# Optimization experiments

Hardware: AMD Instinct MI355X
Metric: run time of the kernel (lower is better)

Reference implementation:

```python
import jax, jax.numpy as jnp
import numpy as np

B, C, W, H, HEADS = 4, 512, 32, 32, 8
D = C // HEADS          # head dim = 64
N = W * H               # tokens = 1024


def setup_inputs() -> dict:
    key = jax.random.key(0)
    ks = jax.random.split(key, 11)
    s = 0.02
    return {
        "q1": jax.random.normal(ks[0], (B, C, W, H), jnp.float32),
        "q2": jax.random.normal(ks[1], (B, C, W, H), jnp.float32),
        "q3": jax.random.normal(ks[2], (B, C, W, H), jnp.float32),
        "Wq": jax.random.normal(ks[3], (C, C), jnp.float32) * s,
        "bq": jnp.zeros((C,), jnp.float32),
        "Wk": jax.random.normal(ks[4], (C, C), jnp.float32) * s,
        "bk": jnp.zeros((C,), jnp.float32),
        "Wv": jax.random.normal(ks[5], (C, C), jnp.float32) * s,
        "bv": jnp.zeros((C,), jnp.float32),
        # BoT-style relative position embeddings (broadcast over the grid)
        "rel_h": jax.random.normal(ks[6], (HEADS, D, 1, H), jnp.float32) * s,
        "rel_w": jax.random.normal(ks[7], (HEADS, D, W, 1), jnp.float32) * s,
    }


def reference(q1, q2, q3, Wq, bq, Wk, bk, Wv, bv, rel_h, rel_w):
    b, c, w, h = q1.shape
    heads = rel_h.shape[0]
    d = c // heads
    n = w * h

    def proj(x, Wm, bm):
        # 1x1 conv == channel matmul; then view (b, heads, d, n)
        y = jnp.einsum('oc,bchw->bohw', Wm, x) + bm[None, :, None, None]
        return y.reshape(b, heads, d, n)

    q = proj(q1, Wq, bq)
    k = proj(q2, Wk, bk)
    v = proj(q3, Wv, bv)

    # (heads, d, w, h) -> (heads, d, n); used transposed as (heads, n, d)
    pos = (rel_h + rel_w).reshape(heads, d, n)

    def branch(a, bmat, outv):
        # energy = a^T bmat + pos^T a ; softmax over last dim; out = outv @ attn^T
        energy = (jnp.einsum('bhdn,bhdm->bhnm', a, bmat)
                  + jnp.einsum('hdn,bhdm->bhnm', pos, a))
        attn = jax.nn.softmax(energy, axis=-1)  # (b, heads, n, n)
        out = jnp.einsum('bhdm,bhnm->bhdn', outv, attn)
        return out.reshape(b, c, w, h)

    out_q = branch(q, k, v)   # energy_q = q^T k + pos^T q ; out = v @ attn_q^T
    out_k = branch(k, v, q)   # energy_k = k^T v + pos^T k ; out = q @ attn_k^T
    out_v = branch(v, q, k)   # energy_v = v^T q + pos^T v ; out = k @ attn_v^T

    return jnp.concatenate((out_q, out_k, out_v), axis=0)
```

## Files before the change

kernel.cpp:

```cpp
#include <hip/hip_runtime.h>

typedef __attribute__((ext_vector_type(8))) __bf16 bf16x8;
typedef __attribute__((ext_vector_type(4))) float f32x4;
typedef __attribute__((ext_vector_type(4))) int i32x4;
typedef __attribute__((ext_vector_type(2))) int i32x2;
typedef __attribute__((ext_vector_type(4))) unsigned short u16x4;
typedef __attribute__((ext_vector_type(8))) unsigned short u16x8;
typedef unsigned short u16;
typedef unsigned int u32;

#define DEVI __device__ __forceinline__

constexpr int CB = 4;
constexpr int CC = 512;
constexpr int CH = 8;
constexpr int CD = 64;
constexpr int CN = 1024;
constexpr float L2E = 1.44269504088896f;

DEVI u16 f2bf(float f) {
    u32 u = __builtin_bit_cast(u32, f);
    u = (u + 0x7FFFu + ((u >> 16) & 1u)) >> 16;
    return (u16)u;
}
DEVI float bf2f(u16 u) {
    return __builtin_bit_cast(float, (u32)u << 16);
}
DEVI u16 f2bf_c(float f) {
    return __builtin_bit_cast(u16, (__bf16)f);
}
DEVI float exp2_fast(float x) {
    float r;
    asm("v_exp_f32 %0, %1" : "=v"(r) : "v"(x));
    return r;
}

DEVI int swzA(int row, int col16) {
    return (row * 256 + col16 * 16) ^ ((row & 7) << 4);
}
DEVI int swzB(int row, int col16) {
    return (row * 128 + col16 * 16) ^ ((row & 7) << 4);
}

DEVI bf16x8 ldfrag(const u16* base, int byteoff) {
    const i32x4* p = reinterpret_cast<const i32x4*>(reinterpret_cast<const char*>(base) + byteoff);
    return __builtin_bit_cast(bf16x8, *p);
}
DEVI void st16(u16* base, int byteoff, i32x4 v) {
    *reinterpret_cast<i32x4*>(reinterpret_cast<char*>(base) + byteoff) = v;
}
DEVI void st8(u16* base, int byteoff, i32x2 v) {
    *reinterpret_cast<i32x2*>(reinterpret_cast<char*>(base) + byteoff) = v;
}
DEVI void async16(u16* lds, const u16* g) {
    __builtin_amdgcn_global_load_lds(
        (const __attribute__((address_space(1))) unsigned int*)g,
        (__attribute__((address_space(3))) unsigned int*)lds,
        16, 0, 0);
}

__global__ __launch_bounds__(256) void mqf_convx_kernel(
    const float* __restrict__ q1, const float* __restrict__ q2, const float* __restrict__ q3,
    u16* __restrict__ XT)
{
    __shared__ u16 T[64 * 66];
    const int t = threadIdx.x;
    const int n0 = blockIdx.x * 64, c0 = blockIdx.y * 64;
    const int p = blockIdx.z >> 2, b = blockIdx.z & 3;
    const float* X = (p == 0 ? q1 : p == 1 ? q2 : q3) + (size_t)b * CC * CN;
    u16* dst = XT + (size_t)(p * CB + b) * CN * CC;

    #pragma unroll
    for (int pass = 0; pass < 4; ++pass) {
        int idx = pass * 256 + t;
        int cl = idx >> 4, nl = (idx & 15) * 4;
        f32x4 v = *reinterpret_cast<const f32x4*>(X + (size_t)(c0 + cl) * CN + n0 + nl);
        u32 lo = (u32)f2bf(v[0]) | ((u32)f2bf(v[1]) << 16);
        u32 hi = (u32)f2bf(v[2]) | ((u32)f2bf(v[3]) << 16);
        *reinterpret_cast<u32*>(&T[cl * 66 + nl]) = lo;
        *reinterpret_cast<u32*>(&T[cl * 66 + nl + 2]) = hi;
    }
    __syncthreads();
    #pragma unroll
    for (int pass = 0; pass < 2; ++pass) {
        int idx = pass * 256 + t;
        int nl = idx >> 3, g = idx & 7;
        u16x8 pk;
        #pragma unroll
        for (int j = 0; j < 8; ++j) pk[j] = T[(g * 8 + j) * 66 + nl];
        *reinterpret_cast<u16x8*>(dst + (size_t)(n0 + nl) * CC + c0 + g * 8) = pk;
    }
}

__global__ __launch_bounds__(256) void mqf_convw_kernel(
    const float* __restrict__ Wq, const float* __restrict__ Wk, const float* __restrict__ Wv,
    u16* __restrict__ Wbf)
{
    int idx = (blockIdx.x * 256 + threadIdx.x) * 4;
    int p = idx >> 18;
    int off = idx & 0x3FFFF;
    const float* W = (p == 0 ? Wq : p == 1 ? Wk : Wv);
    f32x4 v = *reinterpret_cast<const f32x4*>(W + off);
    u16x4 pk;
    #pragma unroll
    for (int j = 0; j < 4; ++j) pk[j] = f2bf(v[j]);
    *reinterpret_cast<u16x4*>(Wbf + idx) = pk;
}

__global__ __launch_bounds__(256) void mqf_gemm_kernel(
    const u16* __restrict__ Wbf, const u16* __restrict__ XT,
    const float* __restrict__ bq, const float* __restrict__ bk, const float* __restrict__ bv,
    u16* __restrict__ projN, u16* __restrict__ projT)
{
    __shared__ __align__(16) u16 At[128 * 64];
    __shared__ __align__(16) u16 Bt[128 * 64];

    const int t = threadIdx.x;
    const int w = t >> 6, l = t & 63;
    const int n0 = blockIdx.x * 128;
    const int o0 = blockIdx.y * 128;
    const int p = blockIdx.z >> 2, b = blockIdx.z & 3;

    const u16* A = Wbf + (size_t)p * CC * CC;
    const u16* B = XT + (size_t)(p * CB + b) * CN * CC;
    const float* bm = (p == 0 ? bq : p == 1 ? bk : bv);
    u16* oN = projN + (size_t)(p * CB + b) * CC * CN;
    u16* oT = projT + (size_t)(p * CB + b) * CN * CC;

    const int srow = t >> 3;
    const int sj = t & 7;

    const f32x4 fz = {0.f, 0.f, 0.f, 0.f};
    f32x4 acc[4][4];
    #pragma unroll
    for (int m = 0; m < 4; ++m)
        #pragma unroll
        for (int s = 0; s < 4; ++s) acc[m][s] = fz;

    const int wr = (w >> 1) * 64;
    const int wc = (w & 1) * 64;

    for (int c0 = 0; c0 < CC; c0 += 64) {
        __syncthreads();
        #pragma unroll
        for (int q = 0; q < 4; ++q) {
            int row = q * 32 + srow;
            int col = (sj ^ (row & 7)) * 8;
            async16(&At[q * 2048 + t * 8], A + (size_t)(o0 + row) * CC + c0 + col);
            async16(&Bt[q * 2048 + t * 8], B + (size_t)(n0 + row) * CC + c0 + col);
        }
        __syncthreads();
        __builtin_amdgcn_s_setprio(1);
        #pragma unroll
        for (int kk = 0; kk < 2; ++kk) {
            bf16x8 af[4], bfr[4];
            #pragma unroll
            for (int m = 0; m < 4; ++m)
                af[m] = ldfrag(At, swzB(wr + m * 16 + (l & 15), kk * 4 + (l >> 4)));
            #pragma unroll
            for (int s = 0; s < 4; ++s)
                bfr[s] = ldfrag(Bt, swzB(wc + s * 16 + (l & 15), kk * 4 + (l >> 4)));
            #pragma unroll
            for (int m = 0; m < 4; ++m)
                #pragma unroll
                for (int s = 0; s < 4; ++s)
                    acc[m][s] = __builtin_amdgcn_mfma_f32_16x16x32_bf16(af[m], bfr[s], acc[m][s], 0, 0, 0);
        }
        __builtin_amdgcn_s_setprio(0);
    }

    #pragma unroll
    for (int m = 0; m < 4; ++m) {
        int obase = o0 + wr + m * 16 + (l >> 4) * 4;
        float bias[4];
        #pragma unroll
        for (int r = 0; r < 4; ++r) bias[r] = bm[obase + r];
        #pragma unroll
        for (int s = 0; s < 4; ++s) {
            int n = n0 + wc + s * 16 + (l & 15);
            u16x4 pk;
            #pragma unroll
            for (int r = 0; r < 4; ++r) {
                float v = acc[m][s][r] + bias[r];
                pk[r] = f2bf(v);
                oN[(size_t)(obase + r) * CN + n] = pk[r];
            }
            *reinterpret_cast<u16x4*>(oT + (size_t)n * CC + obase) = pk;
        }
    }
}

__global__ __launch_bounds__(256, 3) void mqf_attn_kernel(
    const u16* __restrict__ projN, const u16* __restrict__ projT,
    const float* __restrict__ rel_h, const float* __restrict__ rel_w,
    float* __restrict__ out)
{
    __shared__ __align__(16) u16 Kt[2][64 * 128];
    __shared__ __align__(16) u16 Vt[2][64 * 64];

    const int t = threadIdx.x;
    const int w = t >> 6, l = t & 63;
    const int li = l & 15, hi = l >> 4;

    int id = blockIdx.x + (blockIdx.y << 3) + (blockIdx.z << 8);
    int nid = (id & 7) * 96 + (id >> 3);
    const int n0 = (nid & 7) * 128;
    const int by = (nid >> 3) & 31;
    const int br = nid >> 8;
    const int b = by >> 3, h = by & 7;

    const int ai = br, bi = (br + 1) % 3, vi = (br + 2) % 3;
    const size_t tsz = (size_t)CB * CC * CN;
    const u16* aT = projT + ai * tsz + (size_t)b * CN * CC;
    const u16* bT = projT + bi * tsz + (size_t)b * CN * CC;
    const u16* vN = projN + vi * tsz + (size_t)b * CC * CN;

    bf16x8 qf[2][4];
    #pragma unroll
    for (int g = 0; g < 2; ++g) {
        const int nq = n0 + (w * 2 + g) * 16 + li;
        #pragma unroll
        for (int kk = 0; kk < 2; ++kk) {
            u16x8 raw = *reinterpret_cast<const u16x8*>(
                aT + (size_t)nq * CC + h * CD + kk * 32 + hi * 8);
            u16x8 pk;
            #pragma unroll
            for (int j = 0; j < 8; ++j) pk[j] = f2bf_c(bf2f(raw[j]) * L2E);
            qf[g][kk] = __builtin_bit_cast(bf16x8, pk);
        }
        #pragma unroll
        for (int kk = 2; kk < 4; ++kk) {
            u16x8 pk;
            #pragma unroll
            for (int j = 0; j < 8; ++j) {
                int d = (kk - 2) * 32 + hi * 8 + j;
                float f = rel_h[(h * CD + d) * 32 + (nq & 31)]
                        + rel_w[(h * CD + d) * 32 + (nq >> 5)];
                pk[j] = f2bf_c(f * L2E);
            }
            qf[g][kk] = __builtin_bit_cast(bf16x8, pk);
        }
    }

    const f32x4 fz = {0.f, 0.f, 0.f, 0.f};
    f32x4 oacc[2][4];
    #pragma unroll
    for (int g = 0; g < 2; ++g)
        #pragma unroll
        for (int dg = 0; dg < 4; ++dg) oacc[g][dg] = fz;
    float lsum[2] = {0.f, 0.f};

    i32x4 kreg[4], vreg[2];
    const int krow = t >> 2, kc = (t & 3) * 8;
    const int vrow = t >> 3, vc = (t & 7) * 8;
    const int k7 = krow & 7;
    const int vb0 = ((vc >> 5) << 6) + (((vc >> 2) & 3) << 4) + (((vc >> 4) & 1) << 3);

    auto loadKV = [&](int m1) {
        const u16* rb = bT + (size_t)(m1 + krow) * CC + h * CD;
        const u16* ra = aT + (size_t)(m1 + krow) * CC + h * CD;
        kreg[0] = *reinterpret_cast<const i32x4*>(rb + kc);
        kreg[1] = *reinterpret_cast<const i32x4*>(rb + 32 + kc);
        kreg[2] = *reinterpret_cast<const i32x4*>(ra + kc);
        kreg[3] = *reinterpret_cast<const i32x4*>(ra + 32 + kc);
        const u16* rv = vN + (size_t)(h * CD + vrow) * CN + m1;
        vreg[0] = *reinterpret_cast<const i32x4*>(rv + vc);
        vreg[1] = *reinterpret_cast<const i32x4*>(rv + (size_t)32 * CN + vc);
    };
    auto writeKV = [&](u16* KtW, u16* VtW) {
        #pragma unroll
        for (int q = 0; q < 4; ++q) {
            int u = q * 4 + (t & 3);
            st16(KtW, krow * 256 + ((u ^ k7) << 4), kreg[q]);
        }
        i32x2 lo0 = {vreg[0][0], vreg[0][1]}, hi0 = {vreg[0][2], vreg[0][3]};
        int r0 = vrow, r1 = vrow + 32;
        st8(VtW, (r0 * 128 + vb0) ^ ((r0 & 7) << 4), lo0);
        st8(VtW, (r0 * 128 + vb0 + 16) ^ ((r0 & 7) << 4), hi0);
        i32x2 lo1 = {vreg[1][0], vreg[1][1]}, hi1 = {vreg[1][2], vreg[1][3]};
        st8(VtW, (r1 * 128 + vb0) ^ ((r1 & 7) << 4), lo1);
        st8(VtW, (r1 * 128 + vb0 + 16) ^ ((r1 & 7) << 4), hi1);
    };

    loadKV(0);
    writeKV(Kt[0], Vt[0]);
    loadKV(64);
    __syncthreads();

    for (int tt = 0; tt < 16; ++tt) {
        const u16* KtC = Kt[tt & 1];
        const u16* VtC = Vt[tt & 1];
        if (tt < 15) writeKV(Kt[(tt + 1) & 1], Vt[(tt + 1) & 1]);
        if (tt < 14) loadKV((tt + 2) * 64);

        f32x4 e[2][4];
        #pragma unroll
        for (int s = 0; s < 4; ++s) { e[0][s] = fz; e[1][s] = fz; }
        __builtin_amdgcn_s_setprio(1);
        #pragma unroll
        for (int kk = 0; kk < 4; ++kk) {
            #pragma unroll
            for (int s = 0; s < 4; ++s) {
                bf16x8 af = ldfrag(KtC, swzA(s * 16 + li, kk * 4 + hi));
                e[0][s] = __builtin_amdgcn_mfma_f32_16x16x32_bf16(af, qf[0][kk], e[0][s], 0, 0, 0);
                e[1][s] = __builtin_amdgcn_mfma_f32_16x16x32_bf16(af, qf[1][kk], e[1][s], 0, 0, 0);
            }
        }
        __builtin_amdgcn_s_setprio(0);

        bf16x8 pa[2][2];
        #pragma unroll
        for (int g = 0; g < 2; ++g) {
            float ts = 0.f;
            #pragma unroll
            for (int s = 0; s < 4; ++s) {
                #pragma unroll
                for (int r = 0; r < 4; ++r) {
                    float pv = exp2_fast(e[g][s][r]);
                    e[g][s][r] = pv;
                    ts += pv;
                }
            }
            lsum[g] += ts;
            #pragma unroll
            for (int kk = 0; kk < 2; ++kk) {
                u16x8 pk;
                #pragma unroll
                for (int r = 0; r < 4; ++r) {
                    pk[r]     = f2bf_c(e[g][2 * kk][r]);
                    pk[4 + r] = f2bf_c(e[g][2 * kk + 1][r]);
                }
                pa[g][kk] = __builtin_bit_cast(bf16x8, pk);
            }
        }

        __builtin_amdgcn_s_setprio(1);
        #pragma unroll
        for (int kk = 0; kk < 2; ++kk) {
            #pragma unroll
            for (int dg = 0; dg < 4; ++dg) {
                bf16x8 vf = ldfrag(VtC, swzB(dg * 16 + li, kk * 4 + hi));
                oacc[0][dg] = __builtin_amdgcn_mfma_f32_16x16x32_bf16(vf, pa[0][kk], oacc[0][dg], 0, 0, 0);
                oacc[1][dg] = __builtin_amdgcn_mfma_f32_16x16x32_bf16(vf, pa[1][kk], oacc[1][dg], 0, 0, 0);
            }
        }
        __builtin_amdgcn_s_setprio(0);
        __syncthreads();
    }

    #pragma unroll
    for (int g = 0; g < 2; ++g) {
        float lt = lsum[g];
        lt += __shfl_xor(lt, 16, 64);
        lt += __shfl_xor(lt, 32, 64);
        float inv = 1.f / lt;
        float* outp = out + ((size_t)(br * CB + b) * CC + h * CD) * CN
                    + n0 + (w * 2 + g) * 16 + li;
        #pragma unroll
        for (int dg = 0; dg < 4; ++dg) {
            #pragma unroll
            for (int r = 0; r < 4; ++r) {
                int drow = dg * 16 + hi * 4 + r;
                outp[(size_t)drow * CN] = oacc[g][dg][r] * inv;
            }
        }
    }
}

extern "C" void kernel_launch(void* const* d_in, const int* in_sizes, int n_in,
                              void* d_out, int out_size, void* d_ws, size_t ws_size,
                              hipStream_t stream) {
    const float* q1 = (const float*)d_in[0];
    const float* q2 = (const float*)d_in[1];
    const float* q3 = (const float*)d_in[2];
    const float* Wq = (const float*)d_in[3];
    const float* bq = (const float*)d_in[4];
    const float* Wk = (const float*)d_in[5];
    const float* bk = (const float*)d_in[6];
    const float* Wv = (const float*)d_in[7];
    const float* bv = (const float*)d_in[8];
    const float* rh = (const float*)d_in[9];
    const float* rw = (const float*)d_in[10];

    u16* XT    = (u16*)d_ws;
    u16* Wbf   = XT + (size_t)3 * CB * CN * CC;
    u16* projN = Wbf + (size_t)3 * CC * CC;
    u16* projT = projN + (size_t)3 * CB * CC * CN;
    float* outp = (float*)d_out;

    dim3 gc(CN / 64, CC / 64, 12);
    mqf_convx_kernel<<<gc, 256, 0, stream>>>(q1, q2, q3, XT);
    mqf_convw_kernel<<<768, 256, 0, stream>>>(Wq, Wk, Wv, Wbf);
    dim3 gg(CN / 128, CC / 128, 12);
    mqf_gemm_kernel<<<gg, 256, 0, stream>>>(Wbf, XT, bq, bk, bv, projN, projT);
    dim3 ga(CN / 128, CB * CH, 3);
    mqf_attn_kernel<<<ga, 256, 0, stream>>>(projN, projT, rh, rw, outp);
}
```

Baseline: 82.39 us.

## Software-pipeline PV MFMA of previous tile behind current QK and softmax

Splits the K and V staging into separate load/write steps and delays V's shared-memory write by one iteration. The P·V matrix multiply for tile tt-1 is issued right after the QK MFMAs of tile tt, inside the same high-priority region. A final epilogue handles the last tile. The aim is to overlap the exp/convert softmax work with MFMA execution and to shorten the critical path between the two matmul phases. The cost is that the pa fragments stay live across iterations, which raises register pressure.

New measurement: 86.37 us. 1.05x slower.

```diff
diff --git a/kernel.cpp b/kernel.cpp
--- a/kernel.cpp
+++ b/kernel.cpp
@@ -249,6 +249,7 @@
         #pragma unroll
         for (int dg = 0; dg < 4; ++dg) oacc[g][dg] = fz;
     float lsum[2] = {0.f, 0.f};
+    bf16x8 pa[2][2];
 
     i32x4 kreg[4], vreg[2];
     const int krow = t >> 2, kc = (t & 3) * 8;
@@ -256,23 +257,27 @@
     const int k7 = krow & 7;
     const int vb0 = ((vc >> 5) << 6) + (((vc >> 2) & 3) << 4) + (((vc >> 4) & 1) << 3);
 
-    auto loadKV = [&](int m1) {
+    auto loadK = [&](int m1) {
         const u16* rb = bT + (size_t)(m1 + krow) * CC + h * CD;
         const u16* ra = aT + (size_t)(m1 + krow) * CC + h * CD;
         kreg[0] = *reinterpret_cast<const i32x4*>(rb + kc);
         kreg[1] = *reinterpret_cast<const i32x4*>(rb + 32 + kc);
         kreg[2] = *reinterpret_cast<const i32x4*>(ra + kc);
         kreg[3] = *reinterpret_cast<const i32x4*>(ra + 32 + kc);
+    };
+    auto loadV = [&](int m1) {
         const u16* rv = vN + (size_t)(h * CD + vrow) * CN + m1;
         vreg[0] = *reinterpret_cast<const i32x4*>(rv + vc);
         vreg[1] = *reinterpret_cast<const i32x4*>(rv + (size_t)32 * CN + vc);
     };
-    auto writeKV = [&](u16* KtW, u16* VtW) {
+    auto writeK = [&](u16* KtW) {
         #pragma unroll
         for (int q = 0; q < 4; ++q) {
             int u = q * 4 + (t & 3);
             st16(KtW, krow * 256 + ((u ^ k7) << 4), kreg[q]);
         }
+    };
+    auto writeV = [&](u16* VtW) {
         i32x2 lo0 = {vreg[0][0], vreg[0][1]}, hi0 = {vreg[0][2], vreg[0][3]};
         int r0 = vrow, r1 = vrow + 32;
         st8(VtW, (r0 * 128 + vb0) ^ ((r0 & 7) << 4), lo0);
@@ -282,16 +287,19 @@
         st8(VtW, (r1 * 128 + vb0 + 16) ^ ((r1 & 7) << 4), hi1);
     };
 
-    loadKV(0);
-    writeKV(Kt[0], Vt[0]);
-    loadKV(64);
+    loadK(0);
+    loadV(0);
+    writeK(Kt[0]);
+    loadK(64);
     __syncthreads();
 
     for (int tt = 0; tt < 16; ++tt) {
+        writeV(Vt[tt & 1]);
+        if (tt < 15) writeK(Kt[(tt + 1) & 1]);
+        if (tt < 14) loadK((tt + 2) * 64);
+        if (tt < 15) loadV((tt + 1) * 64);
+
         const u16* KtC = Kt[tt & 1];
-        const u16* VtC = Vt[tt & 1];
-        if (tt < 15) writeKV(Kt[(tt + 1) & 1], Vt[(tt + 1) & 1]);
-        if (tt < 14) loadKV((tt + 2) * 64);
 
         f32x4 e[2][4];
         #pragma unroll
@@ -306,9 +314,20 @@
                 e[1][s] = __builtin_amdgcn_mfma_f32_16x16x32_bf16(af, qf[1][kk], e[1][s], 0, 0, 0);
             }
         }
+        if (tt > 0) {
+            const u16* VtP = Vt[(tt - 1) & 1];
+            #pragma unroll
+            for (int kk = 0; kk < 2; ++kk) {
+                #pragma unroll
+                for (int dg = 0; dg < 4; ++dg) {
+                    bf16x8 vf = ldfrag(VtP, swzB(dg * 16 + li, kk * 4 + hi));
+                    oacc[0][dg] = __builtin_amdgcn_mfma_f32_16x16x32_bf16(vf, pa[0][kk], oacc[0][dg], 0, 0, 0);
+                    oacc[1][dg] = __builtin_amdgcn_mfma_f32_16x16x32_bf16(vf, pa[1][kk], oacc[1][dg], 0, 0, 0);
+                }
+            }
+        }
         __builtin_amdgcn_s_setprio(0);
 
-        bf16x8 pa[2][2];
         #pragma unroll
         for (int g = 0; g < 2; ++g) {
             float ts = 0.f;
@@ -333,20 +352,20 @@
                 pa[g][kk] = __builtin_bit_cast(bf16x8, pk);
             }
         }
-
-        __builtin_amdgcn_s_setprio(1);
-        #pragma unroll
-        for (int kk = 0; kk < 2; ++kk) {
-            #pragma unroll
-            for (int dg = 0; dg < 4; ++dg) {
-                bf16x8 vf = ldfrag(VtC, swzB(dg * 16 + li, kk * 4 + hi));
-                oacc[0][dg] = __builtin_amdgcn_mfma_f32_16x16x32_bf16(vf, pa[0][kk], oacc[0][dg], 0, 0, 0);
-                oacc[1][dg] = __builtin_amdgcn_mfma_f32_16x16x32_bf16(vf, pa[1][kk], oacc[1][dg], 0, 0, 0);
-            }
-        }
-        __builtin_amdgcn_s_setprio(0);
         __syncthreads();
     }
+
+    __builtin_amdgcn_s_setprio(1);
+    #pragma unroll
+    for (int kk = 0; kk < 2; ++kk) {
+        #pragma unroll
+        for (int dg = 0; dg < 4; ++dg) {
+            bf16x8 vf = ldfrag(Vt[1], swzB(dg * 16 + li, kk * 4 + hi));
+            oacc[0][dg] = __builtin_amdgcn_mfma_f32_16x16x32_bf16(vf, pa[0][kk], oacc[0][dg], 0, 0, 0);
+            oacc[1][dg] = __builtin_amdgcn_mfma_f32_16x16x32_bf16(vf, pa[1][kk], oacc[1][dg], 0, 0, 0);
+        }
+    }
+    __builtin_amdgcn_s_setprio(0);
 
     #pragma unroll
     for (int g = 0; g < 2; ++g) {
```

## Fold weight conversion into input conversion kernel and DMA K tiles into LDS

Applied to the files above, without the earlier changes.

Removes the separate weight bf16 conversion launch by having half the threads of each input-transpose block convert a slice of the weights. In the attention kernel, K tiles are now loaded with global_load_lds async DMA straight into swizzled shared memory instead of going through registers, leaving only V on the register path. This is meant to cut one kernel launch and reduce register pressure and load/store instructions in the attention loop. The risks are that the DMA completion ordering relative to the existing barriers must be correct, and that the extra work slightly lengthens the convert kernel.

New measurement: 75.72 us. -8.1%, faster.

```diff
diff --git a/kernel.cpp b/kernel.cpp
--- a/kernel.cpp
+++ b/kernel.cpp
@@ -61,7 +61,8 @@
 
 __global__ __launch_bounds__(256) void mqf_convx_kernel(
     const float* __restrict__ q1, const float* __restrict__ q2, const float* __restrict__ q3,
-    u16* __restrict__ XT)
+    const float* __restrict__ Wq, const float* __restrict__ Wk, const float* __restrict__ Wv,
+    u16* __restrict__ XT, u16* __restrict__ Wbf)
 {
     __shared__ u16 T[64 * 66];
     const int t = threadIdx.x;
@@ -69,6 +70,19 @@
     const int p = blockIdx.z >> 2, b = blockIdx.z & 3;
     const float* X = (p == 0 ? q1 : p == 1 ? q2 : q3) + (size_t)b * CC * CN;
     u16* dst = XT + (size_t)(p * CB + b) * CN * CC;
+
+    if (t < 128) {
+        int bid = blockIdx.x + (blockIdx.y << 4) + (blockIdx.z << 7);
+        int idx = (bid * 128 + t) * 4;
+        int pw = idx >> 18;
+        int off = idx & 0x3FFFF;
+        const float* W = (pw == 0 ? Wq : pw == 1 ? Wk : Wv);
+        f32x4 v = *reinterpret_cast<const f32x4*>(W + off);
+        u16x4 pk;
+        #pragma unroll
+        for (int j = 0; j < 4; ++j) pk[j] = f2bf(v[j]);
+        *reinterpret_cast<u16x4*>(Wbf + idx) = pk;
+    }
 
     #pragma unroll
     for (int pass = 0; pass < 4; ++pass) {
@@ -92,21 +106,6 @@
     }
 }
 
-__global__ __launch_bounds__(256) void mqf_convw_kernel(
-    const float* __restrict__ Wq, const float* __restrict__ Wk, const float* __restrict__ Wv,
-    u16* __restrict__ Wbf)
-{
-    int idx = (blockIdx.x * 256 + threadIdx.x) * 4;
-    int p = idx >> 18;
-    int off = idx & 0x3FFFF;
-    const float* W = (p == 0 ? Wq : p == 1 ? Wk : Wv);
-    f32x4 v = *reinterpret_cast<const f32x4*>(W + off);
-    u16x4 pk;
-    #pragma unroll
-    for (int j = 0; j < 4; ++j) pk[j] = f2bf(v[j]);
-    *reinterpret_cast<u16x4*>(Wbf + idx) = pk;
-}
-
 __global__ __launch_bounds__(256) void mqf_gemm_kernel(
     const u16* __restrict__ Wbf, const u16* __restrict__ XT,
     const float* __restrict__ bq, const float* __restrict__ bk, const float* __restrict__ bv,
@@ -250,29 +249,16 @@
         for (int dg = 0; dg < 4; ++dg) oacc[g][dg] = fz;
     float lsum[2] = {0.f, 0.f};
 
-    i32x4 kreg[4], vreg[2];
-    const int krow = t >> 2, kc = (t & 3) * 8;
+    i32x4 vreg[2];
     const int vrow = t >> 3, vc = (t & 7) * 8;
-    const int k7 = krow & 7;
     const int vb0 = ((vc >> 5) << 6) + (((vc >> 2) & 3) << 4) + (((vc >> 4) & 1) << 3);
 
-    auto loadKV = [&](int m1) {
-        const u16* rb = bT + (size_t)(m1 + krow) * CC + h * CD;
-        const u16* ra = aT + (size_t)(m1 + krow) * CC + h * CD;
-        kreg[0] = *reinterpret_cast<const i32x4*>(rb + kc);
-        kreg[1] = *reinterpret_cast<const i32x4*>(rb + 32 + kc);
-        kreg[2] = *reinterpret_cast<const i32x4*>(ra + kc);
-        kreg[3] = *reinterpret_cast<const i32x4*>(ra + 32 + kc);
+    auto loadV = [&](int m1) {
         const u16* rv = vN + (size_t)(h * CD + vrow) * CN + m1;
         vreg[0] = *reinterpret_cast<const i32x4*>(rv + vc);
         vreg[1] = *reinterpret_cast<const i32x4*>(rv + (size_t)32 * CN + vc);
     };
-    auto writeKV = [&](u16* KtW, u16* VtW) {
-        #pragma unroll
-        for (int q = 0; q < 4; ++q) {
-            int u = q * 4 + (t & 3);
-            st16(KtW, krow * 256 + ((u ^ k7) << 4), kreg[q]);
-        }
+    auto writeV = [&](u16* VtW) {
         i32x2 lo0 = {vreg[0][0], vreg[0][1]}, hi0 = {vreg[0][2], vreg[0][3]};
         int r0 = vrow, r1 = vrow + 32;
         st8(VtW, (r0 * 128 + vb0) ^ ((r0 & 7) << 4), lo0);
@@ -281,17 +267,32 @@
         st8(VtW, (r1 * 128 + vb0) ^ ((r1 & 7) << 4), lo1);
         st8(VtW, (r1 * 128 + vb0 + 16) ^ ((r1 & 7) << 4), hi1);
     };
-
-    loadKV(0);
-    writeKV(Kt[0], Vt[0]);
-    loadKV(64);
+    auto issueKdma = [&](int m1, u16* KtW) {
+        #pragma unroll
+        for (int i = 0; i < 4; ++i) {
+            int row = w * 16 + i * 4 + hi;
+            int col16 = li ^ (row & 7);
+            const u16* src = ((li & 8) ? aT : bT)
+                + (size_t)(m1 + row) * CC + h * CD + (col16 & 7) * 8;
+            async16(KtW + w * 2048 + i * 512 + l * 8, src);
+        }
+    };
+
+    loadV(0);
+    writeV(Vt[0]);
+    issueKdma(0, Kt[0]);
+    loadV(64);
     __syncthreads();
 
     for (int tt = 0; tt < 16; ++tt) {
+        if (tt < 15) {
+            writeV(Vt[(tt + 1) & 1]);
+            issueKdma((tt + 1) * 64, Kt[(tt + 1) & 1]);
+        }
+        if (tt < 14) loadV((tt + 2) * 64);
+
         const u16* KtC = Kt[tt & 1];
         const u16* VtC = Vt[tt & 1];
-        if (tt < 15) writeKV(Kt[(tt + 1) & 1], Vt[(tt + 1) & 1]);
-        if (tt < 14) loadKV((tt + 2) * 64);
 
         f32x4 e[2][4];
         #pragma unroll
@@ -389,8 +390,7 @@
     float* outp = (float*)d_out;
 
     dim3 gc(CN / 64, CC / 64, 12);
-    mqf_convx_kernel<<<gc, 256, 0, stream>>>(q1, q2, q3, XT);
-    mqf_convw_kernel<<<768, 256, 0, stream>>>(Wq, Wk, Wv, Wbf);
+    mqf_convx_kernel<<<gc, 256, 0, stream>>>(q1, q2, q3, Wq, Wk, Wv, XT, Wbf);
     dim3 gg(CN / 128, CC / 128, 12);
     mqf_gemm_kernel<<<gg, 256, 0, stream>>>(Wbf, XT, bq, bk, bv, projN, projT);
     dim3 ga(CN / 128, CB * CH, 3);
```
